# Optimization experiments

Measured on AMD Instinct MI355X. Metric: run time of the kernel, lower is better.

The kernel has to match this reference:

```python
import jax, jax.numpy as jnp
import numpy as np

D = 1024   # model dim
H = 16     # heads
HD = D // H
L = 14     # layers
FF = 4096  # ffn hidden
T = 768    # sequence length


def layer_norm(x, g, b, eps):
    m = x.mean(-1, keepdims=True)
    v = ((x - m) ** 2).mean(-1, keepdims=True)
    return (x - m) / jnp.sqrt(v + eps) * g + b


def rel_pos_emb(t, d):
    # EspnetRelPositionalEncoding: concat(flip(pe_positive), pe_negative[1:]) -> (1, 2t-1, d)
    pos = jnp.arange(t, dtype=jnp.float32)
    div = jnp.exp(jnp.arange(0, d, 2, dtype=jnp.float32) * (-jnp.log(10000.0) / d))
    ang = pos[:, None] * div[None, :]                              # (t, d/2)
    pe_pos = jnp.stack([jnp.sin(ang), jnp.cos(ang)], -1).reshape(t, d)
    pe_neg = jnp.stack([jnp.sin(-ang), jnp.cos(-ang)], -1).reshape(t, d)
    return jnp.concatenate([pe_pos[::-1], pe_neg[1:]], 0)[None]    # (1, 2t-1, d)


def rel_shift(x):
    # x: (b, h, t, 2t-1) -> (b, h, t, t), Transformer-XL shift
    b, h, t, n = x.shape
    xp = jnp.concatenate([jnp.zeros((b, h, t, 1), x.dtype), x], -1)  # (b,h,t,n+1)
    xp = xp.reshape(b, h, n + 1, t)
    x = xp[:, :, 1:].reshape(b, h, t, n)
    return x[..., : n // 2 + 1]


def setup_inputs() -> dict:
    key = jax.random.key(0)
    ks = iter(jax.random.split(key, 40))
    s = 0.02
    nrm = lambda k, shape: jax.random.normal(k, shape, dtype=jnp.float32) * s
    return {
        "xs": jax.random.normal(next(ks), (1, T, D), dtype=jnp.float32),
        "embed_W": nrm(next(ks), (D, D)), "embed_b": jnp.zeros((D,), jnp.float32),
        "embed_ln_g": jnp.ones((D,), jnp.float32), "embed_ln_b": jnp.zeros((D,), jnp.float32),
        "Wq": nrm(next(ks), (L, D, D)), "bq": jnp.zeros((L, D), jnp.float32),
        "Wk": nrm(next(ks), (L, D, D)), "bk": jnp.zeros((L, D), jnp.float32),
        "Wv": nrm(next(ks), (L, D, D)), "bv": jnp.zeros((L, D), jnp.float32),
        "Wo": nrm(next(ks), (L, D, D)), "bo": jnp.zeros((L, D), jnp.float32),
        "Wp": nrm(next(ks), (L, D, D)),
        "pos_u": nrm(next(ks), (L, H, HD)), "pos_v": nrm(next(ks), (L, H, HD)),
        "ln1_g": jnp.ones((L, D), jnp.float32), "ln1_b": jnp.zeros((L, D), jnp.float32),
        "ln2_g": jnp.ones((L, D), jnp.float32), "ln2_b": jnp.zeros((L, D), jnp.float32),
        "ff_W1": nrm(next(ks), (L, D, FF)), "ff_b1": jnp.zeros((L, FF), jnp.float32),
        "ff_W2": nrm(next(ks), (L, FF, D)), "ff_b2": jnp.zeros((L, D), jnp.float32),
        "after_g": jnp.ones((D,), jnp.float32), "after_b": jnp.zeros((D,), jnp.float32),
    }


def reference(xs, embed_W, embed_b, embed_ln_g, embed_ln_b,
              Wq, bq, Wk, bk, Wv, bv, Wo, bo, Wp, pos_u, pos_v,
              ln1_g, ln1_b, ln2_g, ln2_b, ff_W1, ff_b1, ff_W2, ff_b2,
              after_g, after_b):
    b, t, _ = xs.shape
    # LegacyLinearNoSubsampling: Linear -> LayerNorm(eps=1e-5) -> (dropout) -> ReLU
    h = jnp.maximum(layer_norm(xs @ embed_W + embed_b, embed_ln_g, embed_ln_b, 1e-5), 0.0)
    x = h * jnp.sqrt(jnp.float32(D))          # pos-enc scale factor
    pos = rel_pos_emb(t, D)                    # (1, 2t-1, D)
    scale = jnp.float32(HD) ** -0.5
    for i in range(L):
        res = x
        xn = layer_norm(x, ln1_g[i], ln1_b[i], 1e-12)
        q = (xn @ Wq[i] + bq[i]).reshape(b, t, H, HD).transpose(0, 2, 1, 3)   # bhtd
        k = (xn @ Wk[i] + bk[i]).reshape(b, t, H, HD).transpose(0, 2, 1, 3)
        v = (xn @ Wv[i] + bv[i]).reshape(b, t, H, HD).transpose(0, 2, 1, 3)
        p = (pos @ Wp[i]).reshape(1, 2 * t - 1, H, HD).transpose(0, 2, 1, 3)  # bhnd
        ac = jnp.einsum('bhtd,bhsd->bhts', q + pos_u[i][None, :, None, :], k)
        bd = rel_shift(jnp.einsum('bhtd,bhnd->bhtn', q + pos_v[i][None, :, None, :], p))
        attn = jax.nn.softmax((ac + bd) * scale, axis=-1)
        o = jnp.einsum('bhts,bhsd->bhtd', attn, v).transpose(0, 2, 1, 3).reshape(b, t, D)
        x = res + (o @ Wo[i] + bo[i])
        res = x
        xn = layer_norm(x, ln2_g[i], ln2_b[i], 1e-12)
        x = res + (jnp.maximum(xn @ ff_W1[i] + ff_b1[i], 0.0) @ ff_W2[i] + ff_b2[i])
    return layer_norm(x, after_g, after_b, 1e-5)
```

## Files before the change

### kernel.cpp

```cpp
#include <hip/hip_runtime.h>
#include <hip/hip_bf16.h>
#include <math.h>

#define D_    1024
#define H_    16
#define HD_   64
#define L_    14
#define FF_   4096
#define T_    768
#define NPOS_ (2*T_-1)

using s16x8  = __attribute__((ext_vector_type(8))) short;
using f32x4  = __attribute__((ext_vector_type(4))) float;
using f32x16 = __attribute__((ext_vector_type(16))) float;

__device__ inline short f2bf(float f) {
  __hip_bfloat16 h = __float2bfloat16(f);
  return *reinterpret_cast<short*>(&h);
}
__device__ inline float bf2f(unsigned short u) {
  union { unsigned u; float f; } v; v.u = ((unsigned)u) << 16; return v.f;
}

__device__ inline float waveRedSum(float v) {
#pragma unroll
  for (int o = 32; o > 0; o >>= 1) v += __shfl_down(v, o, 64);
  return v;
}
__device__ inline float blockRedSum(float v, float* sh) {
  int lane = threadIdx.x & 63, wid = threadIdx.x >> 6;
  v = waveRedSum(v);
  if (lane == 0) sh[wid] = v;
  __syncthreads();
  if (wid == 0) {
    float x = (lane < 4) ? sh[lane] : 0.f;
    x = waveRedSum(x);
    if (lane == 0) sh[0] = x;
  }
  __syncthreads();
  float r = sh[0];
  __syncthreads();
  return r;
}

__global__ __launch_bounds__(256) void ln_kernel(
    const float* __restrict__ x, const float* __restrict__ g,
    const float* __restrict__ b, void* __restrict__ y,
    float eps, int relu, float scale, int obf)
{
  __shared__ float sh[8];
  long row = blockIdx.x;
  const float* xr = x + row * D_;
  int tid = threadIdx.x;
  float4 v = *(const float4*)&xr[tid * 4];
  float s  = v.x + v.y + v.z + v.w;
  float sq = v.x * v.x + v.y * v.y + v.z * v.z + v.w * v.w;
  float mean = blockRedSum(s, sh) * (1.f / D_);
  float esq  = blockRedSum(sq, sh) * (1.f / D_);
  float var  = esq - mean * mean;
  if (var < 0.f) var = 0.f;
  float inv = rsqrtf(var + eps);
  float4 gv = *(const float4*)&g[tid * 4];
  float4 bv = *(const float4*)&b[tid * 4];
  float o0 = (v.x - mean) * inv * gv.x + bv.x;
  float o1 = (v.y - mean) * inv * gv.y + bv.y;
  float o2 = (v.z - mean) * inv * gv.z + bv.z;
  float o3 = (v.w - mean) * inv * gv.w + bv.w;
  if (relu) {
    o0 = fmaxf(o0, 0.f); o1 = fmaxf(o1, 0.f);
    o2 = fmaxf(o2, 0.f); o3 = fmaxf(o3, 0.f);
  }
  o0 *= scale; o1 *= scale; o2 *= scale; o3 *= scale;
  if (obf) {
    short4 sv;
    sv.x = f2bf(o0); sv.y = f2bf(o1); sv.z = f2bf(o2); sv.w = f2bf(o3);
    *(short4*)&((unsigned short*)y)[row * D_ + tid * 4] = sv;
  } else {
    float4 ov; ov.x = o0; ov.y = o1; ov.z = o2; ov.w = o3;
    *(float4*)&((float*)y)[row * D_ + tid * 4] = ov;
  }
}

__global__ __launch_bounds__(256) void transpose_kernel(
    const float* __restrict__ in, unsigned short* __restrict__ out, int K, int N)
{
  __shared__ unsigned short t[32][33];
  long z = blockIdx.z;
  in  += z * (long)K * N;
  out += z * (long)K * N;
  int n0 = blockIdx.x * 32, k0 = blockIdx.y * 32;
  int tid = threadIdx.x;
  int r = tid >> 3, c4 = (tid & 7) * 4;
  float4 v = *(const float4*)&in[(long)(k0 + r) * N + n0 + c4];
  t[r][c4 + 0] = (unsigned short)f2bf(v.x);
  t[r][c4 + 1] = (unsigned short)f2bf(v.y);
  t[r][c4 + 2] = (unsigned short)f2bf(v.z);
  t[r][c4 + 3] = (unsigned short)f2bf(v.w);
  __syncthreads();
  ushort4 s;
  s.x = t[c4 + 0][r]; s.y = t[c4 + 1][r]; s.z = t[c4 + 2][r]; s.w = t[c4 + 3][r];
  *(ushort4*)&out[(long)(n0 + r) * K + k0 + c4] = s;
}

template<int BM, int BN, int WM, int WN, bool CBF16>
__global__ __launch_bounds__(WM * WN * 64) void gemm7_kernel(
    const unsigned short* __restrict__ A, int lda, long sAz,
    const unsigned short* __restrict__ B0, const unsigned short* __restrict__ B1,
    const unsigned short* __restrict__ B2, int ldb, long sBz,
    void* C0, void* C1, void* C2, int ldc, long sCz,
    const float* __restrict__ bias0, const float* __restrict__ bias1,
    const float* __restrict__ bias2,
    const float* __restrict__ resid, int ldres,
    int M, int N, int K, int zPerG, int relu, int nM)
{
  constexpr int NT = WM * WN * 64;
  constexpr int FM = BM / WM / 32;
  constexpr int A_IT = BM * 8 / NT;
  constexpr int B_IT = BN * 8 / NT;

  __shared__ short As[BM * 64];
  __shared__ short Bs[BN * 64];

  int nb = gridDim.x, bid = blockIdx.x;
  int q = nb >> 3, r = nb & 7, xcd = bid & 7, idx = bid >> 3;
  int lbid = (xcd < r ? xcd * (q + 1) : r * (q + 1) + (xcd - r) * q) + idx;
  int mT = lbid % nM, nT = lbid / nM;
  int m0 = mT * BM, n0 = nT * BN;

  int z = blockIdx.z;
  int g = z / zPerG, zb = z - g * zPerG;
  A += (long)zb * sAz;
  const unsigned short* Bh = ((g == 0) ? B0 : ((g == 1) ? B1 : B2)) + zb * sBz;
  void* Cv = (g == 0) ? C0 : ((g == 1) ? C1 : C2);
  const float* bias = (g == 0) ? bias0 : ((g == 1) ? bias1 : bias2);
  float* Cf = (float*)Cv + zb * sCz;
  unsigned short* Ch = (unsigned short*)Cv + zb * sCz;

  int tid = threadIdx.x, lane = tid & 63, wid = tid >> 6;
  int wrow = wid / WN, wcol = wid % WN;
  int wm0 = wrow * (BM / WM), wn0 = wcol * 32;
  int l31 = lane & 31, khalf = lane >> 5;

  f32x16 acc[FM];
#pragma unroll
  for (int i = 0; i < FM; ++i)
#pragma unroll
    for (int rr = 0; rr < 16; ++rr) acc[i][rr] = 0.f;

  for (int k0 = 0; k0 < K; k0 += 64) {
#pragma unroll
    for (int it = 0; it < A_IT; ++it) {
      int f = tid + it * NT;
      int row = f >> 3, c8 = f & 7;
      int gm = m0 + row;
      s16x8 v = {0, 0, 0, 0, 0, 0, 0, 0};
      if (gm < M) v = *(const s16x8*)(A + (long)gm * lda + k0 + c8 * 8);
      *(s16x8*)&As[row * 64 + ((c8 ^ (row & 7)) << 3)] = v;
    }
#pragma unroll
    for (int it = 0; it < B_IT; ++it) {
      int f = tid + it * NT;
      int row = f >> 3, c8 = f & 7;
      s16x8 v = *(const s16x8*)(Bh + (long)(n0 + row) * ldb + k0 + c8 * 8);
      *(s16x8*)&Bs[row * 64 + ((c8 ^ (row & 7)) << 3)] = v;
    }
    __syncthreads();
#pragma unroll
    for (int ks = 0; ks < 4; ++ks) {
      int c8 = ks * 2 + khalf;
      int nrow = wn0 + l31;
      s16x8 b = *(const s16x8*)&Bs[nrow * 64 + ((c8 ^ (nrow & 7)) << 3)];
#pragma unroll
      for (int i = 0; i < FM; ++i) {
        int mrow = wm0 + i * 32 + l31;
        s16x8 a = *(const s16x8*)&As[mrow * 64 + ((c8 ^ (mrow & 7)) << 3)];
        acc[i] = __builtin_amdgcn_mfma_f32_32x32x16_bf16(a, b, acc[i], 0, 0, 0);
      }
    }
    __syncthreads();
  }
  int n = n0 + wn0 + l31;
  float bv = bias ? bias[n] : 0.f;
#pragma unroll
  for (int i = 0; i < FM; ++i) {
#pragma unroll
    for (int reg = 0; reg < 16; ++reg) {
      int m = m0 + wm0 + i * 32 + (reg & 3) + 8 * (reg >> 2) + 4 * khalf;
      if (m < M) {
        float v = acc[i][reg] + bv;
        if (resid) v += resid[(long)m * ldres + n];
        if (relu)  v = fmaxf(v, 0.f);
        if constexpr (CBF16) Ch[(long)m * ldc + n] = (unsigned short)f2bf(v);
        else                 Cf[(long)m * ldc + n] = v;
      }
    }
  }
}

template<int BM, int BN, bool CBF16>
__global__ __launch_bounds__(256) void gemm5_kernel(
    const unsigned short* __restrict__ A, int lda, long sAz,
    const void* __restrict__ B0, const void* __restrict__ B1, const void* __restrict__ B2,
    int ldb, long sBz,
    void* C0, void* C1, void* C2, int ldc, long sCz,
    const float* __restrict__ bias0, const float* __restrict__ bias1,
    const float* __restrict__ bias2,
    const float* __restrict__ resid, int ldres,
    int M, int N, int K, int zPerG, int relu, int nM)
{
  constexpr int FM = BM / 32, FN = BN / 32;
  constexpr int A_IT = BM / 32;
  constexpr int NSH = (BN == 128) ? 7 : 6;

  __shared__ short As[BM * 64];
  __shared__ short Bs[BN * 64];

  int nb = gridDim.x, bid = blockIdx.x;
  int q = nb >> 3, r = nb & 7, xcd = bid & 7, idx = bid >> 3;
  int lbid = (xcd < r ? xcd * (q + 1) : r * (q + 1) + (xcd - r) * q) + idx;
  int mT = lbid % nM, nT = lbid / nM;
  int m0 = mT * BM, n0 = nT * BN;

  int z = blockIdx.z;
  int g = z / zPerG, zb = z - g * zPerG;
  A += (long)zb * sAz;
  const void* Bv = (g == 0) ? B0 : ((g == 1) ? B1 : B2);
  void* Cv       = (g == 0) ? C0 : ((g == 1) ? C1 : C2);
  const float* bias = (g == 0) ? bias0 : ((g == 1) ? bias1 : bias2);
  const float* Bf = (const float*)Bv + zb * sBz;
  float* Cf = (float*)Cv + zb * sCz;
  unsigned short* Ch = (unsigned short*)Cv + zb * sCz;

  int tid = threadIdx.x, lane = tid & 63, wid = tid >> 6;
  int wm0 = (wid >> 1) * (BM / 2), wn0 = (wid & 1) * (BN / 2);
  int lr = lane & 15, kl = (lane >> 4) * 8;

  f32x4 acc[FM][FN];
#pragma unroll
  for (int i = 0; i < FM; ++i)
#pragma unroll
    for (int j = 0; j < FN; ++j)
#pragma unroll
      for (int rr = 0; rr < 4; ++rr) acc[i][j][rr] = 0.f;

  for (int k0 = 0; k0 < K; k0 += 64) {
#pragma unroll
    for (int it = 0; it < A_IT; ++it) {
      int f = tid + it * 256;
      int row = f >> 3, c8 = f & 7;
      int gm = m0 + row;
      s16x8 v = {0, 0, 0, 0, 0, 0, 0, 0};
      if (gm < M) v = *(const s16x8*)(A + (long)gm * lda + k0 + c8 * 8);
      *(s16x8*)&As[row * 64 + ((c8 ^ (row & 7)) << 3)] = v;
    }
    constexpr int B_IT2 = BN / 16;
#pragma unroll
    for (int it = 0; it < B_IT2; ++it) {
      int p = tid + it * 256;
      int n = p & (BN - 1), kq = p >> NSH;
      int gn = n0 + n;
      const float* bp = Bf + (long)(k0 + kq * 4) * ldb + gn;
      short4 s;
      s.x = f2bf(bp[0]); s.y = f2bf(bp[ldb]);
      s.z = f2bf(bp[2 * (long)ldb]); s.w = f2bf(bp[3 * (long)ldb]);
      *(short4*)&Bs[n * 64 + ((kq << 2) ^ ((n & 7) << 3))] = s;
    }
    __syncthreads();
#pragma unroll
    for (int kk = 0; kk < 2; ++kk) {
      s16x8 a[FM], b[FN];
#pragma unroll
      for (int i = 0; i < FM; ++i) {
        int row = wm0 + i * 16 + lr;
        a[i] = *(const s16x8*)&As[row * 64 + ((kk * 32 + kl) ^ ((lr & 7) << 3))];
      }
#pragma unroll
      for (int j = 0; j < FN; ++j) {
        int row = wn0 + j * 16 + lr;
        b[j] = *(const s16x8*)&Bs[row * 64 + ((kk * 32 + kl) ^ ((lr & 7) << 3))];
      }
#pragma unroll
      for (int i = 0; i < FM; ++i)
#pragma unroll
        for (int j = 0; j < FN; ++j)
          acc[i][j] = __builtin_amdgcn_mfma_f32_16x16x32_bf16(a[i], b[j], acc[i][j], 0, 0, 0);
    }
    __syncthreads();
  }
#pragma unroll
  for (int i = 0; i < FM; ++i) {
#pragma unroll
    for (int j = 0; j < FN; ++j) {
      int n = n0 + wn0 + j * 16 + lr;
      float bv = bias ? bias[n] : 0.f;
#pragma unroll
      for (int rr = 0; rr < 4; ++rr) {
        int m = m0 + wm0 + i * 16 + (lane >> 4) * 4 + rr;
        if (m < M) {
          float v = acc[i][j][rr] + bv;
          if (resid) v += resid[(long)m * ldres + n];
          if (relu)  v = fmaxf(v, 0.f);
          if constexpr (CBF16) Ch[(long)m * ldc + n] = (unsigned short)f2bf(v);
          else                 Cf[(long)m * ldc + n] = v;
        }
      }
    }
  }
}

__global__ __launch_bounds__(256) void f2bf_kernel(
    const float* __restrict__ x, unsigned short* __restrict__ y, int n4)
{
  int i = blockIdx.x * 256 + threadIdx.x;
  if (i >= n4) return;
  float4 v = *(const float4*)&x[i * 4];
  short4 s; s.x = f2bf(v.x); s.y = f2bf(v.y); s.z = f2bf(v.z); s.w = f2bf(v.w);
  *(short4*)&y[i * 4] = s;
}

__global__ __launch_bounds__(256) void pos_kernel(unsigned short* __restrict__ pos)
{
  int idx = blockIdx.x * 256 + threadIdx.x;
  if (idx >= NPOS_ * (D_ / 2)) return;
  int n = idx / (D_ / 2), i = idx % (D_ / 2);
  float r = (float)(T_ - 1 - n);
  float div = __expf((float)(2 * i) * (-logf(10000.f) / (float)D_));
  float ang = r * div;
  pos[(long)n * D_ + 2 * i]     = (unsigned short)f2bf(sinf(ang));
  pos[(long)n * D_ + 2 * i + 1] = (unsigned short)f2bf(cosf(ang));
}

__global__ __launch_bounds__(256) void flash_attn_kernel(
    const unsigned short* __restrict__ Q, const unsigned short* __restrict__ K,
    const unsigned short* __restrict__ V, const unsigned short* __restrict__ P,
    const float* __restrict__ posu, const float* __restrict__ posv,
    unsigned short* __restrict__ O)
{
  __shared__ short Ks[64 * 64];
  __shared__ short Vs[64 * 64];
  __shared__ short Ps[96 * 64];
  __shared__ float Grgn[32 * 99];
  __shared__ float mxls[2][32], smls[2][32];

  short* qu = (short*)Grgn;
  short* qv = qu + 32 * 64;
  float* G  = Grgn;
  short* Pf = (short*)Grgn;

  int h = blockIdx.y;
  int t0 = blockIdx.x * 32;
  int tid = threadIdx.x, lane = tid & 63, w = tid >> 6;
  int wr = w >> 1, wc = w & 1;
  int lr = lane & 15, lg = lane >> 4;
  int kl = lg * 8;
  const float* pu = posu + h * HD_;
  const float* pv = posv + h * HD_;

  {
    int row = tid >> 3, c8 = tid & 7;
    s16x8 q8 = *(const s16x8*)(Q + (long)(t0 + row) * D_ + h * HD_ + c8 * 8);
    const unsigned short* qp = (const unsigned short*)&q8;
    s16x8 su, sv;
#pragma unroll
    for (int j = 0; j < 8; ++j) {
      float qf = bf2f(qp[j]);
      su[j] = f2bf(qf + pu[c8 * 8 + j]);
      sv[j] = f2bf(qf + pv[c8 * 8 + j]);
    }
    int sw = row * 64 + ((c8 ^ (row & 7)) << 3);
    *(s16x8*)&qu[sw] = su;
    *(s16x8*)&qv[sw] = sv;
  }
  __syncthreads();
  s16x8 aqu[2], aqv[2];
#pragma unroll
  for (int kk = 0; kk < 2; ++kk) {
    int row = wr * 16 + lr;
    int col = (kk * 32 + kl) ^ ((lr & 7) << 3);
    aqu[kk] = *(const s16x8*)&qu[row * 64 + col];
    aqv[kk] = *(const s16x8*)&qv[row * 64 + col];
  }

  float m_[4], l_[4];
  f32x4 acc_o[2];
#pragma unroll
  for (int rr = 0; rr < 4; ++rr) { m_[rr] = -1e30f; l_[rr] = 0.f; }
#pragma unroll
  for (int j = 0; j < 2; ++j)
#pragma unroll
    for (int rr = 0; rr < 4; ++rr) acc_o[j][rr] = 0.f;

  for (int s0 = 0; s0 < T_; s0 += 64) {
    int base = s0 - t0 + T_ - 32;
    __syncthreads();
#pragma unroll
    for (int it = 0; it < 2; ++it) {
      int f = tid + it * 256;
      int row = f >> 3, c8 = f & 7;
      s16x8 v = *(const s16x8*)(K + (long)(s0 + row) * D_ + h * HD_ + c8 * 8);
      *(s16x8*)&Ks[row * 64 + ((c8 ^ (row & 7)) << 3)] = v;
    }
#pragma unroll
    for (int it = 0; it < 4; ++it) {
      int d = tid & 63, sq = tid >> 6;
      int s = it * 16 + sq * 4;
      const unsigned short* vp = V + (long)(s0 + s) * D_ + h * HD_ + d;
      short4 sv4;
      sv4.x = (short)vp[0];
      sv4.y = (short)vp[D_];
      sv4.z = (short)vp[2 * D_];
      sv4.w = (short)vp[3 * D_];
      *(short4*)&Vs[d * 64 + (s ^ ((d & 7) << 3))] = sv4;
    }
#pragma unroll
    for (int it = 0; it < 3; ++it) {
      int f = tid + it * 256;
      int row = f >> 3, c8 = f & 7;
      int gp = base + row; if (gp > NPOS_ - 1) gp = NPOS_ - 1;
      s16x8 v = *(const s16x8*)(P + (long)gp * D_ + h * HD_ + c8 * 8);
      *(s16x8*)&Ps[row * 64 + ((c8 ^ (row & 7)) << 3)] = v;
    }
    __syncthreads();
    f32x4 a_ac[2], a_g[3];
#pragma unroll
    for (int j = 0; j < 2; ++j)
#pragma unroll
      for (int rr = 0; rr < 4; ++rr) a_ac[j][rr] = 0.f;
#pragma unroll
    for (int j = 0; j < 3; ++j)
#pragma unroll
      for (int rr = 0; rr < 4; ++rr) a_g[j][rr] = 0.f;
#pragma unroll
    for (int j = 0; j < 2; ++j)
#pragma unroll
      for (int kk = 0; kk < 2; ++kk) {
        int row = wc * 32 + j * 16 + lr;
        s16x8 b = *(const s16x8*)&Ks[row * 64 + ((kk * 32 + kl) ^ ((lr & 7) << 3))];
        a_ac[j] = __builtin_amdgcn_mfma_f32_16x16x32_bf16(aqu[kk], b, a_ac[j], 0, 0, 0);
      }
#pragma unroll
    for (int j = 0; j < 3; ++j)
#pragma unroll
      for (int kk = 0; kk < 2; ++kk) {
        int row = wc * 48 + j * 16 + lr;
        s16x8 b = *(const s16x8*)&Ps[row * 64 + ((kk * 32 + kl) ^ ((lr & 7) << 3))];
        a_g[j] = __builtin_amdgcn_mfma_f32_16x16x32_bf16(aqv[kk], b, a_g[j], 0, 0, 0);
      }
#pragma unroll
    for (int j = 0; j < 3; ++j)
#pragma unroll
      for (int rr = 0; rr < 4; ++rr) {
        int row = wr * 16 + lg * 4 + rr;
        int col = wc * 48 + j * 16 + lr;
        G[row * 99 + col] = a_g[j][rr];
      }
    __syncthreads();
    float sreg[2][4], pm[4];
#pragma unroll
    for (int rr = 0; rr < 4; ++rr) {
      int row = wr * 16 + lg * 4 + rr;
#pragma unroll
      for (int j = 0; j < 2; ++j) {
        int c = wc * 32 + j * 16 + lr;
        int gc = c - row + 31;
        sreg[j][rr] = (a_ac[j][rr] + G[row * 99 + gc]) * 0.125f;
      }
      pm[rr] = fmaxf(sreg[0][rr], sreg[1][rr]);
    }
#pragma unroll
    for (int o = 1; o < 16; o <<= 1)
#pragma unroll
      for (int rr = 0; rr < 4; ++rr) pm[rr] = fmaxf(pm[rr], __shfl_xor(pm[rr], o, 64));
    if (lr == 0) {
#pragma unroll
      for (int rr = 0; rr < 4; ++rr) mxls[wc][wr * 16 + lg * 4 + rr] = pm[rr];
    }
    __syncthreads();
    float ps[4];
#pragma unroll
    for (int rr = 0; rr < 4; ++rr) {
      int row = wr * 16 + lg * 4 + rr;
      float mnew = fmaxf(m_[rr], fmaxf(mxls[0][row], mxls[1][row]));
      float sc = __expf(m_[rr] - mnew);
      m_[rr] = mnew;
      l_[rr] *= sc;
      acc_o[0][rr] *= sc;
      acc_o[1][rr] *= sc;
      float p0 = __expf(sreg[0][rr] - mnew);
      float p1 = __expf(sreg[1][rr] - mnew);
      ps[rr] = p0 + p1;
      int c0 = wc * 32 + lr, c1 = wc * 32 + 16 + lr;
      ((unsigned short*)Pf)[row * 64 + (c0 ^ ((row & 7) << 3))] = (unsigned short)f2bf(p0);
      ((unsigned short*)Pf)[row * 64 + (c1 ^ ((row & 7) << 3))] = (unsigned short)f2bf(p1);
    }
#pragma unroll
    for (int o = 1; o < 16; o <<= 1)
#pragma unroll
      for (int rr = 0; rr < 4; ++rr) ps[rr] += __shfl_xor(ps[rr], o, 64);
    if (lr == 0) {
#pragma unroll
      for (int rr = 0; rr < 4; ++rr) smls[wc][wr * 16 + lg * 4 + rr] = ps[rr];
    }
    __syncthreads();
#pragma unroll
    for (int rr = 0; rr < 4; ++rr) {
      int row = wr * 16 + lg * 4 + rr;
      l_[rr] += smls[0][row] + smls[1][row];
    }
    s16x8 ap[2];
#pragma unroll
    for (int kk = 0; kk < 2; ++kk) {
      int row = wr * 16 + lr;
      ap[kk] = *(const s16x8*)&((unsigned short*)Pf)[row * 64 + ((kk * 32 + kl) ^ ((lr & 7) << 3))];
    }
#pragma unroll
    for (int j = 0; j < 2; ++j)
#pragma unroll
      for (int kk = 0; kk < 2; ++kk) {
        int row = wc * 32 + j * 16 + lr;
        s16x8 b = *(const s16x8*)&Vs[row * 64 + ((kk * 32 + kl) ^ ((lr & 7) << 3))];
        acc_o[j] = __builtin_amdgcn_mfma_f32_16x16x32_bf16(ap[kk], b, acc_o[j], 0, 0, 0);
      }
  }
#pragma unroll
  for (int j = 0; j < 2; ++j)
#pragma unroll
    for (int rr = 0; rr < 4; ++rr) {
      int row = t0 + wr * 16 + lg * 4 + rr;
      int col = h * HD_ + wc * 32 + j * 16 + lr;
      O[(long)row * D_ + col] = (unsigned short)f2bf(acc_o[j][rr] / l_[rr]);
    }
}

extern "C" void kernel_launch(void* const* d_in, const int* in_sizes, int n_in,
                              void* d_out, int out_size, void* d_ws, size_t ws_size,
                              hipStream_t stream) {
  const float* xs       = (const float*)d_in[0];
  const float* embed_W  = (const float*)d_in[1];
  const float* embed_b  = (const float*)d_in[2];
  const float* embed_g  = (const float*)d_in[3];
  const float* embed_bt = (const float*)d_in[4];
  const float* Wq = (const float*)d_in[5];
  const float* bq = (const float*)d_in[6];
  const float* Wk = (const float*)d_in[7];
  const float* bk = (const float*)d_in[8];
  const float* Wv = (const float*)d_in[9];
  const float* bv = (const float*)d_in[10];
  const float* Wo = (const float*)d_in[11];
  const float* bo = (const float*)d_in[12];
  const float* Wp = (const float*)d_in[13];
  const float* pos_u = (const float*)d_in[14];
  const float* pos_v = (const float*)d_in[15];
  const float* ln1_g = (const float*)d_in[16];
  const float* ln1_b = (const float*)d_in[17];
  const float* ln2_g = (const float*)d_in[18];
  const float* ln2_b = (const float*)d_in[19];
  const float* ff_W1 = (const float*)d_in[20];
  const float* ff_b1 = (const float*)d_in[21];
  const float* ff_W2 = (const float*)d_in[22];
  const float* ff_b2 = (const float*)d_in[23];
  const float* after_g = (const float*)d_in[24];
  const float* after_b = (const float*)d_in[25];
  float* out = (float*)d_out;

  char* w = (char*)d_ws;
  auto carve = [&](size_t bytes) { char* p = w; w += (bytes + 255) & ~(size_t)255; return p; };
  float* bufX  = (float*)carve((size_t)T_ * D_ * 4);
  float* bufT  = (float*)carve((size_t)T_ * D_ * 4);
  unsigned short* xsb  = (unsigned short*)carve((size_t)T_ * D_ * 2);
  unsigned short* XNb  = (unsigned short*)carve((size_t)T_ * D_ * 2);
  unsigned short* Qb   = (unsigned short*)carve((size_t)T_ * D_ * 2);
  unsigned short* Kb   = (unsigned short*)carve((size_t)T_ * D_ * 2);
  unsigned short* Vb   = (unsigned short*)carve((size_t)T_ * D_ * 2);
  unsigned short* Ob   = (unsigned short*)carve((size_t)T_ * D_ * 2);
  unsigned short* Hb   = (unsigned short*)carve((size_t)T_ * FF_ * 2);
  unsigned short* posT = (unsigned short*)carve((size_t)(NPOS_ + 16) * D_ * 2);
  unsigned short* Pall = (unsigned short*)carve((size_t)L_ * NPOS_ * D_ * 2);
  size_t szDD = (size_t)D_ * D_;
  unsigned short* embedWt = (unsigned short*)carve(szDD * 2);
  unsigned short* WqT = (unsigned short*)carve((size_t)L_ * szDD * 2);
  unsigned short* WkT = (unsigned short*)carve((size_t)L_ * szDD * 2);
  unsigned short* WvT = (unsigned short*)carve((size_t)L_ * szDD * 2);
  unsigned short* WoT = (unsigned short*)carve((size_t)L_ * szDD * 2);
  unsigned short* WpT = (unsigned short*)carve((size_t)L_ * szDD * 2);
  unsigned short* W1T = (unsigned short*)carve((size_t)L_ * D_ * FF_ * 2);
  unsigned short* W2T = (unsigned short*)carve((size_t)L_ * D_ * FF_ * 2);
  bool fast = ((size_t)(w - (char*)d_ws) <= ws_size);

  {
    int n = NPOS_ * (D_ / 2);
    pos_kernel<<<(n + 255) / 256, 256, 0, stream>>>(posT);
  }
  f2bf_kernel<<<(T_ * D_ / 4 + 255) / 256, 256, 0, stream>>>(xs, xsb, T_ * D_ / 4);

  if (fast) {
    transpose_kernel<<<dim3(32, 32, 1),  256, 0, stream>>>(embed_W, embedWt, D_, D_);
    transpose_kernel<<<dim3(32, 32, L_), 256, 0, stream>>>(Wq, WqT, D_, D_);
    transpose_kernel<<<dim3(32, 32, L_), 256, 0, stream>>>(Wk, WkT, D_, D_);
    transpose_kernel<<<dim3(32, 32, L_), 256, 0, stream>>>(Wv, WvT, D_, D_);
    transpose_kernel<<<dim3(32, 32, L_), 256, 0, stream>>>(Wo, WoT, D_, D_);
    transpose_kernel<<<dim3(32, 32, L_), 256, 0, stream>>>(Wp, WpT, D_, D_);
    transpose_kernel<<<dim3(128, 32, L_), 256, 0, stream>>>(ff_W1, W1T, D_, FF_);
    transpose_kernel<<<dim3(32, 128, L_), 256, 0, stream>>>(ff_W2, W2T, FF_, D_);

    gemm7_kernel<32, 128, 1, 4, false><<<dim3(192, 1, 1), 256, 0, stream>>>(
        xsb, D_, 0, embedWt, nullptr, nullptr, D_, 0,
        bufT, nullptr, nullptr, D_, 0, embed_b, nullptr, nullptr,
        nullptr, 0, T_, D_, D_, 1, 0, 24);
    ln_kernel<<<T_, 256, 0, stream>>>(bufT, embed_g, embed_bt, bufX, 1e-5f, 1, 32.0f, 0);

    gemm7_kernel<128, 64, 2, 2, true><<<dim3(192, 1, 14), 256, 0, stream>>>(
        posT, D_, 0, WpT, nullptr, nullptr, D_, (long)szDD,
        Pall, nullptr, nullptr, D_, (long)NPOS_ * D_, nullptr, nullptr, nullptr,
        nullptr, 0, NPOS_, D_, D_, 14, 0, 12);

    for (int i = 0; i < L_; ++i) {
      ln_kernel<<<T_, 256, 0, stream>>>(bufX, ln1_g + (long)i * D_, ln1_b + (long)i * D_,
                                        XNb, 1e-12f, 0, 1.0f, 1);
      gemm7_kernel<32, 128, 1, 4, true><<<dim3(192, 1, 3), 256, 0, stream>>>(
          XNb, D_, 0, WqT + i * szDD, WkT + i * szDD, WvT + i * szDD, D_, 0,
          Qb, Kb, Vb, D_, 0,
          bq + (long)i * D_, bk + (long)i * D_, bv + (long)i * D_,
          nullptr, 0, T_, D_, D_, 1, 0, 24);
      flash_attn_kernel<<<dim3(T_ / 32, H_), 256, 0, stream>>>(
          Qb, Kb, Vb, Pall + (long)i * NPOS_ * D_,
          pos_u + (long)i * D_, pos_v + (long)i * D_, Ob);
      gemm7_kernel<32, 64, 1, 2, false><<<dim3(384, 1, 1), 128, 0, stream>>>(
          Ob, D_, 0, WoT + i * szDD, nullptr, nullptr, D_, 0,
          bufX, nullptr, nullptr, D_, 0, bo + (long)i * D_, nullptr, nullptr,
          bufX, D_, T_, D_, D_, 1, 0, 24);
      ln_kernel<<<T_, 256, 0, stream>>>(bufX, ln2_g + (long)i * D_, ln2_b + (long)i * D_,
                                        XNb, 1e-12f, 0, 1.0f, 1);
      gemm7_kernel<32, 128, 1, 4, true><<<dim3(768, 1, 1), 256, 0, stream>>>(
          XNb, D_, 0, W1T + (size_t)i * D_ * FF_, nullptr, nullptr, D_, 0,
          Hb, nullptr, nullptr, FF_, 0, ff_b1 + (long)i * FF_, nullptr, nullptr,
          nullptr, 0, T_, FF_, D_, 1, 1, 24);
      gemm7_kernel<32, 64, 1, 2, false><<<dim3(384, 1, 1), 128, 0, stream>>>(
          Hb, FF_, 0, W2T + (size_t)i * D_ * FF_, nullptr, nullptr, FF_, 0,
          bufX, nullptr, nullptr, D_, 0, ff_b2 + (long)i * D_, nullptr, nullptr,
          bufX, D_, T_, FF_, FF_, 1, 0, 24);
    }
  } else {
    gemm5_kernel<32, 128, false><<<dim3(192, 1, 1), 256, 0, stream>>>(
        xsb, D_, 0, embed_W, nullptr, nullptr, D_, 0,
        bufT, nullptr, nullptr, D_, 0, embed_b, nullptr, nullptr,
        nullptr, 0, T_, D_, D_, 1, 0, 24);
    ln_kernel<<<T_, 256, 0, stream>>>(bufT, embed_g, embed_bt, bufX, 1e-5f, 1, 32.0f, 0);

    gemm5_kernel<128, 64, true><<<dim3(192, 1, 14), 256, 0, stream>>>(
        posT, D_, 0, Wp, nullptr, nullptr, D_, (long)szDD,
        Pall, nullptr, nullptr, D_, (long)NPOS_ * D_, nullptr, nullptr, nullptr,
        nullptr, 0, NPOS_, D_, D_, 14, 0, 12);

    for (int i = 0; i < L_; ++i) {
      ln_kernel<<<T_, 256, 0, stream>>>(bufX, ln1_g + (long)i * D_, ln1_b + (long)i * D_,
                                        XNb, 1e-12f, 0, 1.0f, 1);
      gemm5_kernel<32, 128, true><<<dim3(192, 1, 3), 256, 0, stream>>>(
          XNb, D_, 0, Wq + i * szDD, Wk + i * szDD, Wv + i * szDD, D_, 0,
          Qb, Kb, Vb, D_, 0,
          bq + (long)i * D_, bk + (long)i * D_, bv + (long)i * D_,
          nullptr, 0, T_, D_, D_, 1, 0, 24);
      flash_attn_kernel<<<dim3(T_ / 32, H_), 256, 0, stream>>>(
          Qb, Kb, Vb, Pall + (long)i * NPOS_ * D_,
          pos_u + (long)i * D_, pos_v + (long)i * D_, Ob);
      gemm5_kernel<32, 64, false><<<dim3(384, 1, 1), 256, 0, stream>>>(
          Ob, D_, 0, Wo + i * szDD, nullptr, nullptr, D_, 0,
          bufX, nullptr, nullptr, D_, 0, bo + (long)i * D_, nullptr, nullptr,
          bufX, D_, T_, D_, D_, 1, 0, 24);
      ln_kernel<<<T_, 256, 0, stream>>>(bufX, ln2_g + (long)i * D_, ln2_b + (long)i * D_,
                                        XNb, 1e-12f, 0, 1.0f, 1);
      gemm5_kernel<32, 128, true><<<dim3(768, 1, 1), 256, 0, stream>>>(
          XNb, D_, 0, ff_W1 + (size_t)i * D_ * FF_, nullptr, nullptr, FF_, 0,
          Hb, nullptr, nullptr, FF_, 0, ff_b1 + (long)i * FF_, nullptr, nullptr,
          nullptr, 0, T_, FF_, D_, 1, 1, 24);
      gemm5_kernel<32, 64, false><<<dim3(384, 1, 1), 256, 0, stream>>>(
          Hb, FF_, 0, ff_W2 + (size_t)i * D_ * FF_, nullptr, nullptr, D_, 0,
          bufX, nullptr, nullptr, D_, 0, ff_b2 + (long)i * D_, nullptr, nullptr,
          bufX, D_, T_, FF_, FF_, 1, 0, 24);
    }
  }

  ln_kernel<<<T_, 256, 0, stream>>>(bufX, after_g, after_b, out, 1e-5f, 0, 1.0f, 0);
}
```

Baseline: 3.029 ms.

## Double-buffer GEMM LDS with register prefetch and 16x16x32 MFMA tiles

Replaces the single-buffered gemm7 with gemm8. gemm8 prefetches the next K-tile from global memory into registers while the current tile is computed from a second LDS buffer, so each K step needs one barrier instead of two. It also moves from 32x32x16 to 16x16x32 MFMA with a 2x2 wave grid, and the Wo and FF2 GEMMs now launch 256 threads. Five per-layer weight transposes are merged into one launch. The cost is double the LDS footprint and more registers, which may reduce occupancy.

```diff
diff --git a/kernel.cpp b/kernel.cpp
--- a/kernel.cpp
+++ b/kernel.cpp
@@ -10,9 +10,8 @@
 #define T_    768
 #define NPOS_ (2*T_-1)
 
-using s16x8  = __attribute__((ext_vector_type(8))) short;
-using f32x4  = __attribute__((ext_vector_type(4))) float;
-using f32x16 = __attribute__((ext_vector_type(16))) float;
+using s16x8 = __attribute__((ext_vector_type(8))) short;
+using f32x4 = __attribute__((ext_vector_type(4))) float;
 
 __device__ inline short f2bf(float f) {
   __hip_bfloat16 h = __float2bfloat16(f);
@@ -102,8 +101,37 @@
   *(ushort4*)&out[(long)(n0 + r) * K + k0 + c4] = s;
 }
 
-template<int BM, int BN, int WM, int WN, bool CBF16>
-__global__ __launch_bounds__(WM * WN * 64) void gemm7_kernel(
+__global__ __launch_bounds__(256) void transpose5_kernel(
+    const float* __restrict__ W0, const float* __restrict__ W1,
+    const float* __restrict__ W2, const float* __restrict__ W3,
+    const float* __restrict__ W4,
+    unsigned short* __restrict__ O0, unsigned short* __restrict__ O1,
+    unsigned short* __restrict__ O2, unsigned short* __restrict__ O3,
+    unsigned short* __restrict__ O4)
+{
+  __shared__ unsigned short t[32][33];
+  int z = blockIdx.z;
+  int g = z / L_, zi = z % L_;
+  const float* in = (g == 0) ? W0 : (g == 1) ? W1 : (g == 2) ? W2 : (g == 3) ? W3 : W4;
+  unsigned short* out = (g == 0) ? O0 : (g == 1) ? O1 : (g == 2) ? O2 : (g == 3) ? O3 : O4;
+  in  += (long)zi * D_ * D_;
+  out += (long)zi * D_ * D_;
+  int n0 = blockIdx.x * 32, k0 = blockIdx.y * 32;
+  int tid = threadIdx.x;
+  int r = tid >> 3, c4 = (tid & 7) * 4;
+  float4 v = *(const float4*)&in[(long)(k0 + r) * D_ + n0 + c4];
+  t[r][c4 + 0] = (unsigned short)f2bf(v.x);
+  t[r][c4 + 1] = (unsigned short)f2bf(v.y);
+  t[r][c4 + 2] = (unsigned short)f2bf(v.z);
+  t[r][c4 + 3] = (unsigned short)f2bf(v.w);
+  __syncthreads();
+  ushort4 s;
+  s.x = t[c4 + 0][r]; s.y = t[c4 + 1][r]; s.z = t[c4 + 2][r]; s.w = t[c4 + 3][r];
+  *(ushort4*)&out[(long)(n0 + r) * D_ + k0 + c4] = s;
+}
+
+template<int BM, int BN, bool CBF16>
+__global__ __launch_bounds__(256) void gemm8_kernel(
     const unsigned short* __restrict__ A, int lda, long sAz,
     const unsigned short* __restrict__ B0, const unsigned short* __restrict__ B1,
     const unsigned short* __restrict__ B2, int ldb, long sBz,
@@ -113,13 +141,14 @@
     const float* __restrict__ resid, int ldres,
     int M, int N, int K, int zPerG, int relu, int nM)
 {
-  constexpr int NT = WM * WN * 64;
-  constexpr int FM = BM / WM / 32;
-  constexpr int A_IT = BM * 8 / NT;
-  constexpr int B_IT = BN * 8 / NT;
-
-  __shared__ short As[BM * 64];
-  __shared__ short Bs[BN * 64];
+  constexpr int FM = BM / 32, FN = BN / 32;
+  constexpr int A_IT = BM / 32;
+  constexpr int B_IT = BN / 32;
+
+  __shared__ short As0[BM * 64];
+  __shared__ short Bs0[BN * 64];
+  __shared__ short As1[BM * 64];
+  __shared__ short Bs1[BN * 64];
 
   int nb = gridDim.x, bid = blockIdx.x;
   int q = nb >> 3, r = nb & 7, xcd = bid & 7, idx = bid >> 3;
@@ -137,61 +166,103 @@
   unsigned short* Ch = (unsigned short*)Cv + zb * sCz;
 
   int tid = threadIdx.x, lane = tid & 63, wid = tid >> 6;
-  int wrow = wid / WN, wcol = wid % WN;
-  int wm0 = wrow * (BM / WM), wn0 = wcol * 32;
-  int l31 = lane & 31, khalf = lane >> 5;
-
-  f32x16 acc[FM];
+  int wm0 = (wid >> 1) * (BM / 2), wn0 = (wid & 1) * (BN / 2);
+  int lr = lane & 15, kl = (lane >> 4) * 8;
+
+  f32x4 acc[FM][FN];
 #pragma unroll
   for (int i = 0; i < FM; ++i)
 #pragma unroll
-    for (int rr = 0; rr < 16; ++rr) acc[i][rr] = 0.f;
-
-  for (int k0 = 0; k0 < K; k0 += 64) {
+    for (int j = 0; j < FN; ++j)
+#pragma unroll
+      for (int rr = 0; rr < 4; ++rr) acc[i][j][rr] = 0.f;
+
+  s16x8 ar[A_IT], br[B_IT];
+
+  auto loadT = [&](int k0) {
 #pragma unroll
     for (int it = 0; it < A_IT; ++it) {
-      int f = tid + it * NT;
+      int f = tid + it * 256;
       int row = f >> 3, c8 = f & 7;
       int gm = m0 + row;
       s16x8 v = {0, 0, 0, 0, 0, 0, 0, 0};
       if (gm < M) v = *(const s16x8*)(A + (long)gm * lda + k0 + c8 * 8);
-      *(s16x8*)&As[row * 64 + ((c8 ^ (row & 7)) << 3)] = v;
+      ar[it] = v;
     }
 #pragma unroll
     for (int it = 0; it < B_IT; ++it) {
-      int f = tid + it * NT;
+      int f = tid + it * 256;
       int row = f >> 3, c8 = f & 7;
-      s16x8 v = *(const s16x8*)(Bh + (long)(n0 + row) * ldb + k0 + c8 * 8);
-      *(s16x8*)&Bs[row * 64 + ((c8 ^ (row & 7)) << 3)] = v;
-    }
-    __syncthreads();
-#pragma unroll
-    for (int ks = 0; ks < 4; ++ks) {
-      int c8 = ks * 2 + khalf;
-      int nrow = wn0 + l31;
-      s16x8 b = *(const s16x8*)&Bs[nrow * 64 + ((c8 ^ (nrow & 7)) << 3)];
+      br[it] = *(const s16x8*)(Bh + (long)(n0 + row) * ldb + k0 + c8 * 8);
+    }
+  };
+  auto writeT = [&](short* as, short* bs) {
+#pragma unroll
+    for (int it = 0; it < A_IT; ++it) {
+      int f = tid + it * 256;
+      int row = f >> 3, c8 = f & 7;
+      *(s16x8*)&as[row * 64 + ((c8 ^ (row & 7)) << 3)] = ar[it];
+    }
+#pragma unroll
+    for (int it = 0; it < B_IT; ++it) {
+      int f = tid + it * 256;
+      int row = f >> 3, c8 = f & 7;
+      *(s16x8*)&bs[row * 64 + ((c8 ^ (row & 7)) << 3)] = br[it];
+    }
+  };
+  auto compute = [&](const short* as, const short* bs) {
+#pragma unroll
+    for (int kk = 0; kk < 2; ++kk) {
+      s16x8 a[FM], b[FN];
 #pragma unroll
       for (int i = 0; i < FM; ++i) {
-        int mrow = wm0 + i * 32 + l31;
-        s16x8 a = *(const s16x8*)&As[mrow * 64 + ((c8 ^ (mrow & 7)) << 3)];
-        acc[i] = __builtin_amdgcn_mfma_f32_32x32x16_bf16(a, b, acc[i], 0, 0, 0);
-      }
-    }
-    __syncthreads();
-  }
-  int n = n0 + wn0 + l31;
-  float bv = bias ? bias[n] : 0.f;
+        int row = wm0 + i * 16 + lr;
+        a[i] = *(const s16x8*)&as[row * 64 + ((kk * 32 + kl) ^ ((lr & 7) << 3))];
+      }
+#pragma unroll
+      for (int j = 0; j < FN; ++j) {
+        int row = wn0 + j * 16 + lr;
+        b[j] = *(const s16x8*)&bs[row * 64 + ((kk * 32 + kl) ^ ((lr & 7) << 3))];
+      }
+#pragma unroll
+      for (int i = 0; i < FM; ++i)
+#pragma unroll
+        for (int j = 0; j < FN; ++j)
+          acc[i][j] = __builtin_amdgcn_mfma_f32_16x16x32_bf16(a[i], b[j], acc[i][j], 0, 0, 0);
+    }
+  };
+
+  int nt = K / 64;
+  loadT(0);
+  writeT(As0, Bs0);
+  __syncthreads();
+  for (int t = 0; t < nt; t += 2) {
+    loadT((t + 1) * 64);
+    compute(As0, Bs0);
+    writeT(As1, Bs1);
+    __syncthreads();
+    if (t + 2 < nt) loadT((t + 2) * 64);
+    compute(As1, Bs1);
+    if (t + 2 < nt) writeT(As0, Bs0);
+    __syncthreads();
+  }
+
 #pragma unroll
   for (int i = 0; i < FM; ++i) {
 #pragma unroll
-    for (int reg = 0; reg < 16; ++reg) {
-      int m = m0 + wm0 + i * 32 + (reg & 3) + 8 * (reg >> 2) + 4 * khalf;
-      if (m < M) {
-        float v = acc[i][reg] + bv;
-        if (resid) v += resid[(long)m * ldres + n];
-        if (relu)  v = fmaxf(v, 0.f);
-        if constexpr (CBF16) Ch[(long)m * ldc + n] = (unsigned short)f2bf(v);
-        else                 Cf[(long)m * ldc + n] = v;
+    for (int j = 0; j < FN; ++j) {
+      int n = n0 + wn0 + j * 16 + lr;
+      float bv = bias ? bias[n] : 0.f;
+#pragma unroll
+      for (int rr = 0; rr < 4; ++rr) {
+        int m = m0 + wm0 + i * 16 + (lane >> 4) * 4 + rr;
+        if (m < M) {
+          float v = acc[i][j][rr] + bv;
+          if (resid) v += resid[(long)m * ldres + n];
+          if (relu)  v = fmaxf(v, 0.f);
+          if constexpr (CBF16) Ch[(long)m * ldc + n] = (unsigned short)f2bf(v);
+          else                 Cf[(long)m * ldc + n] = v;
+        }
       }
     }
   }
@@ -595,21 +666,18 @@
 
   if (fast) {
     transpose_kernel<<<dim3(32, 32, 1),  256, 0, stream>>>(embed_W, embedWt, D_, D_);
-    transpose_kernel<<<dim3(32, 32, L_), 256, 0, stream>>>(Wq, WqT, D_, D_);
-    transpose_kernel<<<dim3(32, 32, L_), 256, 0, stream>>>(Wk, WkT, D_, D_);
-    transpose_kernel<<<dim3(32, 32, L_), 256, 0, stream>>>(Wv, WvT, D_, D_);
-    transpose_kernel<<<dim3(32, 32, L_), 256, 0, stream>>>(Wo, WoT, D_, D_);
-    transpose_kernel<<<dim3(32, 32, L_), 256, 0, stream>>>(Wp, WpT, D_, D_);
+    transpose5_kernel<<<dim3(32, 32, 5 * L_), 256, 0, stream>>>(
+        Wq, Wk, Wv, Wo, Wp, WqT, WkT, WvT, WoT, WpT);
     transpose_kernel<<<dim3(128, 32, L_), 256, 0, stream>>>(ff_W1, W1T, D_, FF_);
     transpose_kernel<<<dim3(32, 128, L_), 256, 0, stream>>>(ff_W2, W2T, FF_, D_);
 
-    gemm7_kernel<32, 128, 1, 4, false><<<dim3(192, 1, 1), 256, 0, stream>>>(
+    gemm8_kernel<32, 128, false><<<dim3(192, 1, 1), 256, 0, stream>>>(
         xsb, D_, 0, embedWt, nullptr, nullptr, D_, 0,
         bufT, nullptr, nullptr, D_, 0, embed_b, nullptr, nullptr,
         nullptr, 0, T_, D_, D_, 1, 0, 24);
     ln_kernel<<<T_, 256, 0, stream>>>(bufT, embed_g, embed_bt, bufX, 1e-5f, 1, 32.0f, 0);
 
-    gemm7_kernel<128, 64, 2, 2, true><<<dim3(192, 1, 14), 256, 0, stream>>>(
+    gemm8_kernel<128, 64, true><<<dim3(192, 1, 14), 256, 0, stream>>>(
         posT, D_, 0, WpT, nullptr, nullptr, D_, (long)szDD,
         Pall, nullptr, nullptr, D_, (long)NPOS_ * D_, nullptr, nullptr, nullptr,
         nullptr, 0, NPOS_, D_, D_, 14, 0, 12);
@@ -617,7 +685,7 @@
     for (int i = 0; i < L_; ++i) {
       ln_kernel<<<T_, 256, 0, stream>>>(bufX, ln1_g + (long)i * D_, ln1_b + (long)i * D_,
                                         XNb, 1e-12f, 0, 1.0f, 1);
-      gemm7_kernel<32, 128, 1, 4, true><<<dim3(192, 1, 3), 256, 0, stream>>>(
+      gemm8_kernel<32, 128, true><<<dim3(192, 1, 3), 256, 0, stream>>>(
           XNb, D_, 0, WqT + i * szDD, WkT + i * szDD, WvT + i * szDD, D_, 0,
           Qb, Kb, Vb, D_, 0,
           bq + (long)i * D_, bk + (long)i * D_, bv + (long)i * D_,
@@ -625,17 +693,17 @@
       flash_attn_kernel<<<dim3(T_ / 32, H_), 256, 0, stream>>>(
           Qb, Kb, Vb, Pall + (long)i * NPOS_ * D_,
           pos_u + (long)i * D_, pos_v + (long)i * D_, Ob);
-      gemm7_kernel<32, 64, 1, 2, false><<<dim3(384, 1, 1), 128, 0, stream>>>(
+      gemm8_kernel<32, 64, false><<<dim3(384, 1, 1), 256, 0, stream>>>(
           Ob, D_, 0, WoT + i * szDD, nullptr, nullptr, D_, 0,
           bufX, nullptr, nullptr, D_, 0, bo + (long)i * D_, nullptr, nullptr,
           bufX, D_, T_, D_, D_, 1, 0, 24);
       ln_kernel<<<T_, 256, 0, stream>>>(bufX, ln2_g + (long)i * D_, ln2_b + (long)i * D_,
                                         XNb, 1e-12f, 0, 1.0f, 1);
-      gemm7_kernel<32, 128, 1, 4, true><<<dim3(768, 1, 1), 256, 0, stream>>>(
+      gemm8_kernel<32, 128, true><<<dim3(768, 1, 1), 256, 0, stream>>>(
           XNb, D_, 0, W1T + (size_t)i * D_ * FF_, nullptr, nullptr, D_, 0,
           Hb, nullptr, nullptr, FF_, 0, ff_b1 + (long)i * FF_, nullptr, nullptr,
           nullptr, 0, T_, FF_, D_, 1, 1, 24);
-      gemm7_kernel<32, 64, 1, 2, false><<<dim3(384, 1, 1), 128, 0, stream>>>(
+      gemm8_kernel<32, 64, false><<<dim3(384, 1, 1), 256, 0, stream>>>(
           Hb, FF_, 0, W2T + (size_t)i * D_ * FF_, nullptr, nullptr, FF_, 0,
           bufX, nullptr, nullptr, D_, 0, ff_b2 + (long)i * D_, nullptr, nullptr,
           bufX, D_, T_, FF_, FF_, 1, 0, 24);
```

Result: faster. 2.442 ms (median of 2 runs) (-19.4%).
